# Kernel optimization log

Measured on AMD Instinct MI355X. Metric: run time of the kernel, lower is better.

Reference implementation:

```python
import jax, jax.numpy as jnp
import numpy as np

B, S, H = 16, 2048, 1024
NEG_INF = -10000000.0


def setup_inputs() -> dict:
    key = jax.random.key(0)
    ks = jax.random.split(key, 9)
    s = 1.0 / np.sqrt(H)
    return {
        "queries": jax.random.normal(ks[0], (B, S, H), jnp.float32),
        "keys": jax.random.normal(ks[1], (B, S, H), jnp.float32),
        "values": jax.random.normal(ks[2], (B, S, H), jnp.float32),
        "Wq": jax.random.normal(ks[3], (H, H), jnp.float32) * s,
        "bq": jnp.zeros((H,), jnp.float32),
        "Wk": jax.random.normal(ks[4], (H, H), jnp.float32) * s,
        "bk": jnp.zeros((H,), jnp.float32),
        "Wv": jax.random.normal(ks[5], (H, H), jnp.float32) * s,
        "bv": jnp.zeros((H,), jnp.float32),
    }


def reference(queries, keys, values, Wq, bq, Wk, bk, Wv, bv):
    scale = jax.lax.rsqrt(jnp.float32(H))
    q = jnp.einsum('bsh,oh->bso', queries, Wq) + bq  # (B,S,H)
    k = jnp.einsum('bsh,oh->bso', keys, Wk) + bk
    v = jnp.einsum('bsh,oh->bso', values, Wv) + bv
    scores = jnp.einsum('bqh,bkh->bqk', q, k) * scale  # (B,S,S)
    # Faithful to original: mask = NEG_INF * triu(ones) with diagonal=0,
    # so the diagonal is masked too; softmax over dim=1 (query axis).
    mask = NEG_INF * jnp.triu(jnp.ones((S, S), jnp.float32))
    attn = jax.nn.softmax(scores + mask, axis=1)  # normalize over query dim, as in torch Softmax(dim=1)
    context = jnp.einsum('bqk,bkh->bqh', attn, v)  # (B,S,H)
    return (context, attn)
```

## Files before the change

kernel.cpp:

```cpp
#include <hip/hip_runtime.h>
#include <hip/hip_bf16.h>
#include <stdint.h>

#define B_ 16
#define S_ 2048
#define H_ 1024
static constexpr float NEG_INF_F = -10000000.0f;
static constexpr float SCALE_F   = 0.03125f;

#define BM 256
#define BN 256
#define BK 64
#define HALF_BYTES 16384
#define OPBUF_BYTES 32768

typedef __attribute__((ext_vector_type(4))) float  f32x4;
typedef __attribute__((ext_vector_type(8))) short  bf16x8;
typedef __attribute__((ext_vector_type(4))) short  s16x4;

__device__ __forceinline__ short f2bf(float f) {
  uint32_t u = __float_as_uint(f);
  u = (u + 0x7FFFu + ((u >> 16) & 1u)) >> 16;
  return (short)u;
}

__device__ __forceinline__ void gload16(const void* g, void* l) {
  __builtin_amdgcn_global_load_lds(
      (const __attribute__((address_space(1))) unsigned int*)g,
      (__attribute__((address_space(3))) unsigned int*)l, 16, 0, 0);
}

__device__ __forceinline__ bf16x8 lds_frag(const char* buf, int r, int k) {
  int byte = ((r >> 7) << 14) + ((r & 127) << 7) + (k << 1);
  byte ^= (r & 7) << 4;
  return *(const bf16x8*)(buf + byte);
}

__device__ __forceinline__ void stage_half(const short* __restrict__ rows0,
                                           int ld, int kt, char* dst) {
  const int t = threadIdx.x, w = t >> 6, l = t & 63;
  #pragma unroll
  for (int j = 0; j < 2; ++j) {
    const int idx16 = j * 512 + w * 64 + l;
    const int r  = idx16 >> 3;
    const int cs = ((l & 7) << 4) ^ ((r & 7) << 4);
    gload16(rows0 + (size_t)r * ld + kt + (cs >> 1),
            dst + (size_t)(j * 512 + w * 64) * 16);
  }
}

template<int MODE>
__device__ __forceinline__ void gemm_core256(
    const short* __restrict__ A, const short* __restrict__ Bm,
    const float* __restrict__ bias, void* __restrict__ Cp,
    int K, int lda, int ldb, int ldc, int z, long long strC,
    int row0, int col0, int bx, char* lds, float2* __restrict__ partials) {
  char* ldsA = lds;
  char* ldsB = lds + 2 * OPBUF_BYTES;
  const int lane = threadIdx.x & 63;
  const int wid  = threadIdx.x >> 6;
  const int wm = wid >> 2;
  const int wn = wid & 3;
  const int lr = lane & 15;
  const int lk = (lane >> 4) << 3;

  int kmain = K;
  if constexpr (MODE == 3) { int km = (bx + 1) * BM; kmain = km < K ? km : K; }
  const int ntm = kmain / BK;
  const int nt  = ntm + ((MODE == 3 && kmain < K) ? 1 : 0);

  f32x4 acc[8][4] = {};

  const short* Arows0 = A + (size_t)row0 * lda;
  const short* Arows1 = Arows0 + (size_t)128 * lda;
  const short* Brows0 = Bm + (size_t)col0 * ldb;
  const short* Brows1 = Brows0 + (size_t)128 * ldb;

  auto stage_tile = [&](int buf, int kt) {
    stage_half(Brows0, ldb, kt, ldsB + buf * OPBUF_BYTES);
    stage_half(Brows1, ldb, kt, ldsB + buf * OPBUF_BYTES + HALF_BYTES);
    stage_half(Arows0, lda, kt, ldsA + buf * OPBUF_BYTES);
    stage_half(Arows1, lda, kt, ldsA + buf * OPBUF_BYTES + HALF_BYTES);
  };

  stage_tile(0, 0);
  asm volatile("s_waitcnt vmcnt(0)" ::: "memory");
  __builtin_amdgcn_s_barrier();

  for (int i = 0; i < nt; ++i) {
    const int c = i & 1;
    const char* bA = ldsA + c * OPBUF_BYTES;
    const char* bB = ldsB + c * OPBUF_BYTES;
    if (i + 1 < nt) {
      const int ktn = (i + 1 < ntm) ? (i + 1) * BK : K - BK;
      stage_tile(c ^ 1, ktn);
    }

    bf16x8 bfr[4][2];
    #pragma unroll
    for (int q = 0; q < 4; ++q) {
      if (q == 0) {
        #pragma unroll
        for (int nf = 0; nf < 4; ++nf)
          #pragma unroll
          for (int ks = 0; ks < 2; ++ks)
            bfr[nf][ks] = lds_frag(bB, wn * 64 + nf * 16 + lr, ks * 32 + lk);
      }
      bf16x8 af[2][2];
      #pragma unroll
      for (int fm = 0; fm < 2; ++fm)
        #pragma unroll
        for (int ks = 0; ks < 2; ++ks)
          af[fm][ks] = lds_frag(bA, wm * 128 + q * 32 + fm * 16 + lr, ks * 32 + lk);
      asm volatile("s_waitcnt lgkmcnt(0)" ::: "memory");
      __builtin_amdgcn_sched_barrier(0);
      __builtin_amdgcn_s_setprio(1);
      #pragma unroll
      for (int fm = 0; fm < 2; ++fm)
        #pragma unroll
        for (int nf = 0; nf < 4; ++nf)
          #pragma unroll
          for (int ks = 0; ks < 2; ++ks)
            acc[q * 2 + fm][nf] = __builtin_amdgcn_mfma_f32_16x16x32_bf16(
                af[fm][ks], bfr[nf][ks], acc[q * 2 + fm][nf], 0, 0, 0);
      __builtin_amdgcn_s_setprio(0);
      if (q < 3) __builtin_amdgcn_s_barrier();
    }
    asm volatile("s_waitcnt vmcnt(0)" ::: "memory");
    __builtin_amdgcn_s_barrier();
  }

  float pm[4] = {-3.0e38f, -3.0e38f, -3.0e38f, -3.0e38f};

  #pragma unroll
  for (int mf = 0; mf < 8; ++mf) {
    #pragma unroll
    for (int nf = 0; nf < 4; ++nf) {
      const int mb = row0 + wm * 128 + mf * 16 + ((lane >> 4) << 2);
      const int n  = col0 + wn * 64 + nf * 16 + lr;
      f32x4 a = acc[mf][nf];
      if constexpr (MODE == 0) {
        short* out = (short*)Cp;
        const float bv = bias[n];
        #pragma unroll
        for (int r = 0; r < 4; ++r)
          out[(size_t)(mb + r) * ldc + n] = f2bf(a[r] + bv);
      } else if constexpr (MODE == 1) {
        const float bv = bias[n];
        const int bb = mb >> 11;
        const int ss = mb & (S_ - 1);
        s16x4 pk;
        #pragma unroll
        for (int r = 0; r < 4; ++r) pk[r] = f2bf(a[r] + bv);
        *(s16x4*)((short*)Cp + ((size_t)bb * H_ + n) * S_ + ss) = pk;
      } else if constexpr (MODE == 2) {
        float* out = (float*)Cp + (size_t)z * strC;
        #pragma unroll
        for (int r = 0; r < 4; ++r) {
          const int mrow = mb + r;
          float v = a[r] * SCALE_F + (n >= mrow ? NEG_INF_F : 0.0f);
          out[(size_t)mrow * ldc + n] = v;
          pm[nf] = fmaxf(pm[nf], v);
        }
      } else {
        float* out = (float*)Cp + (size_t)z * strC;
        #pragma unroll
        for (int r = 0; r < 4; ++r)
          out[(size_t)(mb + r) * ldc + n] = a[r];
      }
    }
  }

  if constexpr (MODE == 2) {
    float ps[4] = {0.0f, 0.0f, 0.0f, 0.0f};
    #pragma unroll
    for (int mf = 0; mf < 8; ++mf)
      #pragma unroll
      for (int nf = 0; nf < 4; ++nf) {
        const int mb = row0 + wm * 128 + mf * 16 + ((lane >> 4) << 2);
        const int n  = col0 + wn * 64 + nf * 16 + lr;
        f32x4 a = acc[mf][nf];
        #pragma unroll
        for (int r = 0; r < 4; ++r) {
          float v = a[r] * SCALE_F + (n >= mb + r ? NEG_INF_F : 0.0f);
          ps[nf] += __expf(v - pm[nf]);
        }
      }
    float* smx = (float*)lds;
    float* sse = smx + 512;
    #pragma unroll
    for (int nf = 0; nf < 4; ++nf) {
      float m = pm[nf], s = ps[nf];
      #pragma unroll
      for (int d = 16; d < 64; d <<= 1) {
        float om = __shfl_xor(m, d);
        float os = __shfl_xor(s, d);
        float nm = fmaxf(m, om);
        s = s * __expf(m - nm) + os * __expf(om - nm);
        m = nm;
      }
      if ((lane >> 4) == 0) {
        smx[wm * 256 + wn * 64 + nf * 16 + lr] = m;
        sse[wm * 256 + wn * 64 + nf * 16 + lr] = s;
      }
    }
    __syncthreads();
    if (threadIdx.x < 256) {
      const int col = threadIdx.x;
      float m0 = smx[col], m1 = smx[256 + col];
      float s0 = sse[col], s1 = sse[256 + col];
      float mm = fmaxf(m0, m1);
      float ss = s0 * __expf(m0 - mm) + s1 * __expf(m1 - mm);
      float2 pv; pv.x = mm; pv.y = ss;
      partials[((size_t)z * 8 + (row0 >> 8)) * S_ + col0 + col] = pv;
    }
  }
}

struct ProjArgs {
  const short *xq, *xk, *xv, *wq, *wk, *wv;
  const float *bq, *bk, *bv;
  short *oq, *ok, *ov;
};

__launch_bounds__(512, 1)
__global__ void proj_qk(ProjArgs p) {
  __shared__ char lds[4 * OPBUF_BYTES];
  const int bid = blockIdx.x + (blockIdx.y << 2) + (blockIdx.z << 9);
  const int s = (bid & 7) * 128 + (bid >> 3);
  const int z = s >> 9;
  const int y = (s & 511) >> 2;
  const int x = s & 3;
  if (z == 0)
    gemm_core256<0>(p.xq, p.wq, p.bq, p.oq, H_, H_, H_, H_, 0, 0LL,
                    y * BM, x * BN, x, lds, nullptr);
  else
    gemm_core256<0>(p.xk, p.wk, p.bk, p.ok, H_, H_, H_, H_, 0, 0LL,
                    y * BM, x * BN, x, lds, nullptr);
}

__launch_bounds__(512, 1)
__global__ void proj_v(ProjArgs p) {
  __shared__ char lds[4 * OPBUF_BYTES];
  const int bid = blockIdx.x + (blockIdx.y << 2);
  const int s = (bid & 7) * 64 + (bid >> 3);
  const int y = s >> 2;
  const int x = s & 3;
  gemm_core256<1>(p.xv, p.wv, p.bv, p.ov, H_, H_, H_, 0, 0, 0LL,
                  y * BM, x * BN, x, lds, nullptr);
}

__launch_bounds__(512, 1)
__global__ void scores_k(const short* __restrict__ Qb, const short* __restrict__ Kb,
                         float* __restrict__ attn, float2* __restrict__ partials) {
  const int bid = blockIdx.x + (blockIdx.y << 3) + (blockIdx.z << 6);
  const int s = (bid & 7) * 128 + (bid >> 3);
  const int bz = s >> 6;
  const int by = (s >> 3) & 7;
  const int bx = s & 7;
  if (by > bx && by != 7) return;
  __shared__ char lds[4 * OPBUF_BYTES];
  const size_t zo = (size_t)bz * S_ * H_;
  gemm_core256<2>(Qb + zo, Kb + zo, nullptr, attn, H_, H_, H_, S_, bz,
                  (long long)S_ * S_, bx * BM, by * BN, bx, lds, partials);
}

__launch_bounds__(512, 1)
__global__ void ctx_k(const short* __restrict__ attn_b, const short* __restrict__ Vt,
                      float* __restrict__ ctx) {
  const int bid = blockIdx.x + (blockIdx.y << 3) + (blockIdx.z << 5);
  const int chunk = bid & 7;
  const int r = bid >> 3;
  const int g = r >> 3;
  const int bx = (r < 32) ? (7 - g) : (g - 4);
  const int low = r & 7;
  const int by = low & 3;
  const int bz = chunk * 2 + (low >> 2);
  __shared__ char lds[4 * OPBUF_BYTES];
  gemm_core256<3>(attn_b + (size_t)bz * S_ * S_, Vt + (size_t)bz * H_ * S_,
                  nullptr, ctx, S_, S_, S_, H_, bz, (long long)S_ * H_,
                  bx * BM, by * BN, bx, lds, nullptr);
}

__launch_bounds__(256)
__global__ void cvt6(const float* __restrict__ q, const float* __restrict__ k,
                     const float* __restrict__ v, const float* __restrict__ wq,
                     const float* __restrict__ wk, const float* __restrict__ wv,
                     short* __restrict__ xq, short* __restrict__ xk,
                     short* __restrict__ xv, short* __restrict__ wqb,
                     short* __restrict__ wkb, short* __restrict__ wvb) {
  const int y = blockIdx.y;
  const int stride = gridDim.x * 256;
  if (y < 3) {
    const float* s = (y == 0) ? q : (y == 1) ? k : v;
    short* d       = (y == 0) ? xq : (y == 1) ? xk : xv;
    const int n4 = (B_ * S_ * H_) / 4;
    for (int i = blockIdx.x * 256 + threadIdx.x; i < n4; i += stride) {
      f32x4 x = ((const f32x4*)s)[i];
      s16x4 o;
      #pragma unroll
      for (int j = 0; j < 4; ++j) o[j] = f2bf(x[j]);
      ((s16x4*)d)[i] = o;
    }
  } else {
    const int w4 = (H_ * H_) / 4;
    for (int i = blockIdx.x * 256 + threadIdx.x; i < 3 * w4; i += stride) {
      const int wsel = i >> 18;
      const int j = i & (w4 - 1);
      const float* s = (wsel == 0) ? wq : (wsel == 1) ? wk : wv;
      short* d       = (wsel == 0) ? wqb : (wsel == 1) ? wkb : wvb;
      f32x4 x = ((const f32x4*)s)[j];
      s16x4 o;
      #pragma unroll
      for (int jj = 0; jj < 4; ++jj) o[jj] = f2bf(x[jj]);
      ((s16x4*)d)[j] = o;
    }
  }
}

__launch_bounds__(256)
__global__ void softmax_col(float* __restrict__ attn, short* __restrict__ attn_b,
                            const float2* __restrict__ partials) {
  const int b  = blockIdx.y;
  const int t  = threadIdx.x;
  const int cg = t & 7;
  const int qo = t >> 3;
  const int k0 = blockIdx.x * 32 + cg * 4;
  float* base = attn + (size_t)b * S_ * S_;
  short* bb   = attn_b + (size_t)b * S_ * S_;
  const bool full = (k0 == S_ - 4);

  __shared__ f32x4 bM[8], bI[8];
  if (qo == 0) {
    const int by = k0 >> 8;
    const int bxlo = (by == 7) ? 0 : by;
    f32x4 M4, Sm;
    #pragma unroll
    for (int i = 0; i < 4; ++i) { M4[i] = -3.0e38f; Sm[i] = 0.0f; }
    for (int bx = bxlo; bx < 8; ++bx) {
      const float2* p = partials + ((size_t)b * 8 + bx) * S_ + k0;
      #pragma unroll
      for (int i = 0; i < 4; ++i) {
        float2 pv = p[i];
        float nm = fmaxf(M4[i], pv.x);
        Sm[i] = Sm[i] * __expf(M4[i] - nm) + pv.y * __expf(pv.x - nm);
        M4[i] = nm;
      }
    }
    f32x4 inv;
    #pragma unroll
    for (int i = 0; i < 4; ++i) inv[i] = 1.0f / Sm[i];
    bM[cg] = M4;
    bI[cg] = inv;
  }
  __syncthreads();
  const f32x4 M4  = bM[cg];
  const f32x4 inv = bI[cg];

  const bool zkeep = ((k0 >> 8) == 0) || (k0 >= S_ - 64);
  (void)zkeep;

  for (int q = qo; q < S_; q += 32) {
    const size_t off = (size_t)q * S_ + k0;
    if (full || q > k0) {
      f32x4 x = *(const f32x4*)&base[off];
      f32x4 r;
      s16x4 rb;
      #pragma unroll
      for (int i = 0; i < 4; ++i) { r[i] = __expf(x[i] - M4[i]) * inv[i]; rb[i] = f2bf(r[i]); }
      *(f32x4*)&base[off] = r;
      *(s16x4*)&bb[off]   = rb;
    } else {
      f32x4 zr;
      #pragma unroll
      for (int i = 0; i < 4; ++i) zr[i] = 0.0f;
      *(f32x4*)&base[off] = zr;
      if (((q >> 8) == (k0 >> 8)) || (k0 >= S_ - 64)) {
        s16x4 zb;
        #pragma unroll
        for (int i = 0; i < 4; ++i) zb[i] = 0;
        *(s16x4*)&bb[off] = zb;
      }
    }
  }
}

extern "C" void kernel_launch(void* const* d_in, const int* in_sizes, int n_in,
                              void* d_out, int out_size, void* d_ws, size_t ws_size,
                              hipStream_t stream) {
  const float* queries = (const float*)d_in[0];
  const float* keys    = (const float*)d_in[1];
  const float* values  = (const float*)d_in[2];
  const float* Wq = (const float*)d_in[3];
  const float* bq = (const float*)d_in[4];
  const float* Wk = (const float*)d_in[5];
  const float* bk = (const float*)d_in[6];
  const float* Wv = (const float*)d_in[7];
  const float* bv = (const float*)d_in[8];

  float* ctx  = (float*)d_out;
  float* attn = ctx + (size_t)B_ * S_ * H_;

  short* Qb = (short*)d_ws;
  short* Kb = Qb + (size_t)B_ * S_ * H_;
  short* Vt = Kb + (size_t)B_ * S_ * H_;
  short* attn_b = Qb;

  short* Wqb = (short*)ctx;
  short* Wkb = Wqb + (size_t)H_ * H_;
  short* Wvb = Wkb + (size_t)H_ * H_;
  float2* partials = (float2*)(Wvb + (size_t)H_ * H_);
  short* Xq = (short*)attn;
  short* Xk = Xq + (size_t)B_ * S_ * H_;
  short* Xv = Xk + (size_t)B_ * S_ * H_;

  cvt6<<<dim3(2048, 4, 1), dim3(256, 1, 1), 0, stream>>>(queries, keys, values,
                                                         Wq, Wk, Wv,
                                                         Xq, Xk, Xv, Wqb, Wkb, Wvb);

  ProjArgs pa{Xq, Xk, Xv, Wqb, Wkb, Wvb, bq, bk, bv, Qb, Kb, Vt};
  proj_qk<<<dim3(H_ / BN, 32768 / BM, 2), dim3(512, 1, 1), 0, stream>>>(pa);
  proj_v<<<dim3(H_ / BN, 32768 / BM, 1), dim3(512, 1, 1), 0, stream>>>(pa);

  scores_k<<<dim3(S_ / BM, S_ / BN, B_), dim3(512, 1, 1), 0, stream>>>(Qb, Kb, attn, partials);

  softmax_col<<<dim3(S_ / 32, B_, 1), dim3(256, 1, 1), 0, stream>>>(attn, attn_b, partials);

  ctx_k<<<dim3(S_ / BM, H_ / BN, B_), dim3(512, 1, 1), 0, stream>>>(attn_b, Vt, ctx);
}
```

Before: 798.4 us.

## Fuse fp32-to-bf16 activation conversion into projection GEMM A-operand staging

After: 879.3 us. 10.1% more time.

```diff
diff --git a/kernel.cpp b/kernel.cpp
--- a/kernel.cpp
+++ b/kernel.cpp
@@ -51,10 +51,11 @@
 
 template<int MODE>
 __device__ __forceinline__ void gemm_core256(
-    const short* __restrict__ A, const short* __restrict__ Bm,
+    const void* __restrict__ Ap, const short* __restrict__ Bm,
     const float* __restrict__ bias, void* __restrict__ Cp,
     int K, int lda, int ldb, int ldc, int z, long long strC,
     int row0, int col0, int bx, char* lds, float2* __restrict__ partials) {
+  constexpr bool AF32 = (MODE <= 1);
   char* ldsA = lds;
   char* ldsB = lds + 2 * OPBUF_BYTES;
   const int lane = threadIdx.x & 63;
@@ -64,27 +65,65 @@
   const int lr = lane & 15;
   const int lk = (lane >> 4) << 3;
 
+  const short* A16 = (const short*)Ap;
+  const float* A32 = (const float*)Ap;
+
   int kmain = K;
   if constexpr (MODE == 3) { int km = (bx + 1) * BM; kmain = km < K ? km : K; }
   const int ntm = kmain / BK;
   const int nt  = ntm + ((MODE == 3 && kmain < K) ? 1 : 0);
 
   f32x4 acc[8][4] = {};
-
-  const short* Arows0 = A + (size_t)row0 * lda;
+  f32x4 areg[8];
+
+  const short* Arows0 = A16 + (size_t)row0 * lda;
   const short* Arows1 = Arows0 + (size_t)128 * lda;
   const short* Brows0 = Bm + (size_t)col0 * ldb;
   const short* Brows1 = Brows0 + (size_t)128 * ldb;
 
-  auto stage_tile = [&](int buf, int kt) {
+  auto stage_B = [&](int buf, int kt) {
     stage_half(Brows0, ldb, kt, ldsB + buf * OPBUF_BYTES);
     stage_half(Brows1, ldb, kt, ldsB + buf * OPBUF_BYTES + HALF_BYTES);
+  };
+  auto stage_tile16 = [&](int buf, int kt) {
+    stage_B(buf, kt);
     stage_half(Arows0, lda, kt, ldsA + buf * OPBUF_BYTES);
     stage_half(Arows1, lda, kt, ldsA + buf * OPBUF_BYTES + HALF_BYTES);
   };
-
-  stage_tile(0, 0);
-  asm volatile("s_waitcnt vmcnt(0)" ::: "memory");
+  auto loadA = [&](int kt) {
+    const float* src = A32 + (size_t)(row0 + (threadIdx.x >> 1)) * lda + kt
+                       + ((threadIdx.x & 1) << 5);
+    #pragma unroll
+    for (int g = 0; g < 8; ++g) areg[g] = *(const f32x4*)(src + g * 4);
+  };
+  auto writeA = [&](int buf) {
+    const int r = threadIdx.x >> 1;
+    char* dstA = ldsA + buf * OPBUF_BYTES + ((r >> 7) ? HALF_BYTES : 0)
+                 + ((r & 127) << 7);
+    const int base = (threadIdx.x & 1) << 6;
+    #pragma unroll
+    for (int ci = 0; ci < 4; ++ci) {
+      bf16x8 w;
+      #pragma unroll
+      for (int j = 0; j < 4; ++j) {
+        w[j]     = f2bf(areg[ci * 2][j]);
+        w[j + 4] = f2bf(areg[ci * 2 + 1][j]);
+      }
+      const int inner = (base + ci * 16) ^ ((r & 7) << 4);
+      *(bf16x8*)(dstA + inner) = w;
+    }
+  };
+
+  if constexpr (AF32) {
+    loadA(0);
+    stage_B(0, 0);
+    asm volatile("s_waitcnt vmcnt(0)" ::: "memory");
+    writeA(0);
+    asm volatile("s_waitcnt lgkmcnt(0)" ::: "memory");
+  } else {
+    stage_tile16(0, 0);
+    asm volatile("s_waitcnt vmcnt(0)" ::: "memory");
+  }
   __builtin_amdgcn_s_barrier();
 
   for (int i = 0; i < nt; ++i) {
@@ -93,7 +132,8 @@
     const char* bB = ldsB + c * OPBUF_BYTES;
     if (i + 1 < nt) {
       const int ktn = (i + 1 < ntm) ? (i + 1) * BK : K - BK;
-      stage_tile(c ^ 1, ktn);
+      if constexpr (AF32) { loadA(ktn); stage_B(c ^ 1, ktn); }
+      else stage_tile16(c ^ 1, ktn);
     }
 
     bf16x8 bfr[4][2];
@@ -127,6 +167,10 @@
       if (q < 3) __builtin_amdgcn_s_barrier();
     }
     asm volatile("s_waitcnt vmcnt(0)" ::: "memory");
+    if constexpr (AF32) {
+      if (i + 1 < nt) writeA(c ^ 1);
+      asm volatile("s_waitcnt lgkmcnt(0)" ::: "memory");
+    }
     __builtin_amdgcn_s_barrier();
   }
 
@@ -218,7 +262,8 @@
 }
 
 struct ProjArgs {
-  const short *xq, *xk, *xv, *wq, *wk, *wv;
+  const float *xq, *xk, *xv;
+  const short *wq, *wk, *wv;
   const float *bq, *bk, *bv;
   short *oq, *ok, *ov;
 };
@@ -283,38 +328,21 @@
 }
 
 __launch_bounds__(256)
-__global__ void cvt6(const float* __restrict__ q, const float* __restrict__ k,
-                     const float* __restrict__ v, const float* __restrict__ wq,
-                     const float* __restrict__ wk, const float* __restrict__ wv,
-                     short* __restrict__ xq, short* __restrict__ xk,
-                     short* __restrict__ xv, short* __restrict__ wqb,
+__global__ void cvtW(const float* __restrict__ wq, const float* __restrict__ wk,
+                     const float* __restrict__ wv, short* __restrict__ wqb,
                      short* __restrict__ wkb, short* __restrict__ wvb) {
-  const int y = blockIdx.y;
+  const int w4 = (H_ * H_) / 4;
   const int stride = gridDim.x * 256;
-  if (y < 3) {
-    const float* s = (y == 0) ? q : (y == 1) ? k : v;
-    short* d       = (y == 0) ? xq : (y == 1) ? xk : xv;
-    const int n4 = (B_ * S_ * H_) / 4;
-    for (int i = blockIdx.x * 256 + threadIdx.x; i < n4; i += stride) {
-      f32x4 x = ((const f32x4*)s)[i];
-      s16x4 o;
-      #pragma unroll
-      for (int j = 0; j < 4; ++j) o[j] = f2bf(x[j]);
-      ((s16x4*)d)[i] = o;
-    }
-  } else {
-    const int w4 = (H_ * H_) / 4;
-    for (int i = blockIdx.x * 256 + threadIdx.x; i < 3 * w4; i += stride) {
-      const int wsel = i >> 18;
-      const int j = i & (w4 - 1);
-      const float* s = (wsel == 0) ? wq : (wsel == 1) ? wk : wv;
-      short* d       = (wsel == 0) ? wqb : (wsel == 1) ? wkb : wvb;
-      f32x4 x = ((const f32x4*)s)[j];
-      s16x4 o;
-      #pragma unroll
-      for (int jj = 0; jj < 4; ++jj) o[jj] = f2bf(x[jj]);
-      ((s16x4*)d)[j] = o;
-    }
+  for (int i = blockIdx.x * 256 + threadIdx.x; i < 3 * w4; i += stride) {
+    const int wsel = i >> 18;
+    const int j = i & (w4 - 1);
+    const float* s = (wsel == 0) ? wq : (wsel == 1) ? wk : wv;
+    short* d       = (wsel == 0) ? wqb : (wsel == 1) ? wkb : wvb;
+    f32x4 x = ((const f32x4*)s)[j];
+    s16x4 o;
+    #pragma unroll
+    for (int jj = 0; jj < 4; ++jj) o[jj] = f2bf(x[jj]);
+    ((s16x4*)d)[j] = o;
   }
 }
 
@@ -356,9 +384,6 @@
   __syncthreads();
   const f32x4 M4  = bM[cg];
   const f32x4 inv = bI[cg];
-
-  const bool zkeep = ((k0 >> 8) == 0) || (k0 >= S_ - 64);
-  (void)zkeep;
 
   for (int q = qo; q < S_; q += 32) {
     const size_t off = (size_t)q * S_ + k0;
@@ -410,15 +435,10 @@
   short* Wkb = Wqb + (size_t)H_ * H_;
   short* Wvb = Wkb + (size_t)H_ * H_;
   float2* partials = (float2*)(Wvb + (size_t)H_ * H_);
-  short* Xq = (short*)attn;
-  short* Xk = Xq + (size_t)B_ * S_ * H_;
-  short* Xv = Xk + (size_t)B_ * S_ * H_;
-
-  cvt6<<<dim3(2048, 4, 1), dim3(256, 1, 1), 0, stream>>>(queries, keys, values,
-                                                         Wq, Wk, Wv,
-                                                         Xq, Xk, Xv, Wqb, Wkb, Wvb);
-
-  ProjArgs pa{Xq, Xk, Xv, Wqb, Wkb, Wvb, bq, bk, bv, Qb, Kb, Vt};
+
+  cvtW<<<dim3(768, 1, 1), dim3(256, 1, 1), 0, stream>>>(Wq, Wk, Wv, Wqb, Wkb, Wvb);
+
+  ProjArgs pa{queries, keys, values, Wqb, Wkb, Wvb, bq, bk, bv, Qb, Kb, Vt};
   proj_qk<<<dim3(H_ / BN, 32768 / BM, 2), dim3(512, 1, 1), 0, stream>>>(pa);
   proj_v<<<dim3(H_ / BN, 32768 / BM, 1), dim3(512, 1, 1), 0, stream>>>(pa);
 
```
